# Kernel optimization log

Hardware: AMD Instinct MI355X
Metric: run time of the kernel (lower is better)

## Reference

```python
import jax, jax.numpy as jnp
import numpy as np

EPS = 1e-5  # torch BatchNorm2d default eps
NUM_PIXELS = 2  # M_Relax window
GROUPS = 4


def conv2d(x, w, b, groups, pad):
    y = jax.lax.conv_general_dilated(
        x, w, window_strides=(1, 1), padding=[(pad, pad), (pad, pad)],
        dimension_numbers=('NCHW', 'OIHW', 'NCHW'), feature_group_count=groups)
    return y + b[None, :, None, None]


def batchnorm(x, gamma, beta):
    # training-mode BN: batch statistics over (N,H,W)
    mean = jnp.mean(x, axis=(0, 2, 3), keepdims=True)
    var = jnp.var(x, axis=(0, 2, 3), keepdims=True)
    return gamma[None, :, None, None] * (x - mean) * jax.lax.rsqrt(var + EPS) + beta[None, :, None, None]


def resb(x, w1, b1, w2, b2):
    y = conv2d(x, w1, b1, GROUPS, 1)
    y = jnp.where(y > 0, y, 0.1 * y)  # LeakyReLU(0.1)
    y = conv2d(y, w2, b2, GROUPS, 1)
    return y + x


def m_relax(M, n=NUM_PIXELS):
    # sum of M shifted by -n..n along the query (row) axis with zero padding
    out = M
    for i in range(1, n + 1):
        out = out + jnp.pad(M[:, :-i, :], ((0, 0), (i, 0), (0, 0)))
        out = out + jnp.pad(M[:, i:, :], ((0, 0), (0, i), (0, 0)))
    return out


def reference(x_left, x_right, bn_gamma, bn_beta, rb_w1, rb_b1, rb_w2, rb_b2, q_w, q_b, k_w, k_b):
    b, c, h, w = x_left.shape
    Q = conv2d(resb(batchnorm(x_left, bn_gamma, bn_beta), rb_w1, rb_b1, rb_w2, rb_b2), q_w, q_b, GROUPS, 0)
    K = conv2d(resb(batchnorm(x_right, bn_gamma, bn_beta), rb_w1, rb_b1, rb_w2, rb_b2), k_w, k_b, GROUPS, 0)
    Q = Q - jnp.mean(Q, axis=3, keepdims=True)
    K = K - jnp.mean(K, axis=3, keepdims=True)
    # rows of each image attend across width: [b*h, w, c]
    Qr = Q.transpose(0, 2, 3, 1).reshape(b * h, w, c)
    Kr = K.transpose(0, 2, 3, 1).reshape(b * h, w, c)
    score = jnp.einsum('nuc,nvc->nuv', Qr, Kr)  # [b*h, w, w]
    M_rl = jax.nn.softmax(score, axis=-1)               # right->left
    M_lr = jax.nn.softmax(score.transpose(0, 2, 1), axis=-1)  # left->right
    # validity maps (detached in original)
    V_left = jax.lax.stop_gradient(jnp.einsum('nuv,nvu->nu', m_relax(M_rl), M_lr)).reshape(b, 1, h, w)
    V_right = jax.lax.stop_gradient(jnp.einsum('nuv,nvu->nu', m_relax(M_lr), M_rl)).reshape(b, 1, h, w)
    Vl = jnp.tanh(5.0 * V_left)
    Vr = jnp.tanh(5.0 * V_right)
    xr_rows = x_right.transpose(0, 2, 3, 1).reshape(b * h, w, c)
    xl_rows = x_left.transpose(0, 2, 3, 1).reshape(b * h, w, c)
    x_leftT = jnp.einsum('nuv,nvc->nuc', M_rl, xr_rows).reshape(b, h, w, c).transpose(0, 3, 1, 2)
    x_rightT = jnp.einsum('nuv,nvc->nuc', M_lr, xl_rows).reshape(b, h, w, c).transpose(0, 3, 1, 2)
    out_left = x_left * (1 - Vl) + x_leftT * Vl
    out_right = x_right * (1 - Vr) + x_rightT * Vr
    return out_left, out_right


def setup_inputs() -> dict:
    key = jax.random.key(0)
    ks = jax.random.split(key, 12)
    b, c, h, w = 8, 64, 128, 128
    cg = c // GROUPS
    s_conv3 = 0.1
    return {
        'x_left': jax.random.normal(ks[0], (b, c, h, w), jnp.float32),
        'x_right': jax.random.normal(ks[1], (b, c, h, w), jnp.float32),
        'bn_gamma': jnp.ones((c,), jnp.float32),
        'bn_beta': jnp.zeros((c,), jnp.float32),
        'rb_w1': jax.random.normal(ks[2], (c, cg, 3, 3), jnp.float32) * s_conv3,
        'rb_b1': jax.random.normal(ks[3], (c,), jnp.float32) * 0.01,
        'rb_w2': jax.random.normal(ks[4], (c, cg, 3, 3), jnp.float32) * s_conv3,
        'rb_b2': jax.random.normal(ks[5], (c,), jnp.float32) * 0.01,
        'q_w': jax.random.normal(ks[6], (c, cg, 1, 1), jnp.float32) * 0.2,
        'q_b': jax.random.normal(ks[7], (c,), jnp.float32) * 0.01,
        'k_w': jax.random.normal(ks[8], (c, cg, 1, 1), jnp.float32) * 0.2,
        'k_b': jax.random.normal(ks[9], (c,), jnp.float32) * 0.01,
    }
```

## Files before the change

kernel.cpp:

```cpp
#include <hip/hip_runtime.h>

#define CH_N 64
#define HH 128
#define WW 128
#define BB 8
#define HW (HH*WW)

__global__ __launch_bounds__(256) void k_stats(const float* __restrict__ xL,
                                               const float* __restrict__ xR,
                                               float* __restrict__ sums) {
  int blk = blockIdx.x;
  int img = blk >> 8, c = (blk >> 2) & 63, s = blk & 3;
  const float* x = img ? xR : xL;
  float sm = 0.f, sq = 0.f;
  for (int n = 2*s; n < 2*s+2; ++n) {
    const float4* p = (const float4*)(x + ((size_t)(n*64+c))*HW);
    for (int i = threadIdx.x; i < 4096; i += 256) {
      float4 v = p[i];
      sm += (v.x+v.y)+(v.z+v.w);
      sq += (v.x*v.x+v.y*v.y)+(v.z*v.z+v.w*v.w);
    }
  }
  #pragma unroll
  for (int o = 32; o > 0; o >>= 1) { sm += __shfl_down(sm, o); sq += __shfl_down(sq, o); }
  __shared__ float rs[2][4];
  int wid = threadIdx.x >> 6;
  if ((threadIdx.x & 63) == 0) { rs[0][wid] = sm; rs[1][wid] = sq; }
  __syncthreads();
  if (threadIdx.x == 0) {
    sm = (rs[0][0]+rs[0][1])+(rs[0][2]+rs[0][3]);
    sq = (rs[1][0]+rs[1][1])+(rs[1][2]+rs[1][3]);
    atomicAdd(&sums[(img*64+c)*2+0], sm);
    atomicAdd(&sums[(img*64+c)*2+1], sq);
  }
}

__global__ __launch_bounds__(128) void k_finalize(const float* __restrict__ sums,
                                                  const float* __restrict__ gamma,
                                                  const float* __restrict__ beta,
                                                  float* __restrict__ ss) {
  int t = threadIdx.x;
  if (t < 128) {
    int c = t & 63;
    float sm = sums[t*2], sq = sums[t*2+1];
    float mean = sm * (1.f/131072.f);
    float var  = sq * (1.f/131072.f) - mean*mean;
    float scale = gamma[c] * rsqrtf(var + 1e-5f);
    ss[t*2+0] = scale;
    ss[t*2+1] = beta[c] - mean*scale;
  }
}

#define WOFF  5760
#define QWOFF 4224
#define QBOFF 4480

template<int MODE>
__global__ __launch_bounds__(256, 4) void k_conv(
    const float* __restrict__ inL, const float* __restrict__ inR,
    const float* __restrict__ xresL, const float* __restrict__ xresR,
    const float* __restrict__ w, const float* __restrict__ bias,
    const float* __restrict__ ss,
    float* __restrict__ outL_, float* __restrict__ outR_,
    const float* __restrict__ qwL, const float* __restrict__ qbL,
    const float* __restrict__ qwR, const float* __restrict__ qbR,
    float* __restrict__ rsL, float* __restrict__ rsR) {
  __shared__ float smem[8832];
  int tile = blockIdx.x, g = blockIdx.y, nz = blockIdx.z;
  int img = nz >> 3, n = nz & 7;
  const float* in   = img ? inR : inL;
  const float* xres = img ? xresR : xresL;
  const float* ssp  = ss + img*128;
  float* out        = img ? outR_ : outL_;
  const float* qw1  = img ? qwR : qwL;
  const float* qb1  = img ? qbR : qbL;
  float* rowsum     = img ? rsR : rsL;

  int x0 = (tile & 7) << 4, y0 = (tile >> 3) << 4;
  int t = threadIdx.x;

  {
    int ocw = t >> 4, icw = t & 15;
    const float* wp = w + (size_t)(g*16 + ocw)*144 + icw*9;
    float* wd = &smem[WOFF + ocw*192 + icw*12];
    #pragma unroll
    for (int k = 0; k < 9; ++k) wd[k] = wp[k];
  }

  {
    int p0 = t, p1 = t + 256;
    int ry0 = p0 / 18, rx0 = p0 - ry0*18;
    int gy0 = y0 - 1 + ry0, gx0 = x0 - 1 + rx0;
    bool ok0 = ((unsigned)gy0 < 128u) && ((unsigned)gx0 < 128u);
    int gy0c = gy0 < 0 ? 0 : (gy0 > 127 ? 127 : gy0);
    int gx0c = gx0 < 0 ? 0 : (gx0 > 127 ? 127 : gx0);
    const float* sp0 = in + ((size_t)(n*64 + g*16)*128 + gy0c)*128 + gx0c;
    float* dp0 = &smem[ry0*20 + rx0];

    bool two = (p1 < 324);
    int ry1 = p1 / 18, rx1 = p1 - ry1*18;
    int gy1 = y0 - 1 + ry1, gx1 = x0 - 1 + rx1;
    bool ok1 = ((unsigned)gy1 < 128u) && ((unsigned)gx1 < 128u);
    int gy1c = gy1 < 0 ? 0 : (gy1 > 127 ? 127 : gy1);
    int gx1c = gx1 < 0 ? 0 : (gx1 > 127 ? 127 : gx1);
    const float* sp1 = in + ((size_t)(n*64 + g*16)*128 + gy1c)*128 + gx1c;
    float* dp1 = &smem[ry1*20 + rx1];

    #pragma unroll
    for (int ic = 0; ic < 16; ++ic) {
      float sA = 0.f, sB = 0.f;
      if (MODE == 0) { sA = ssp[(g*16+ic)*2]; sB = ssp[(g*16+ic)*2+1]; }
      float v0 = sp0[(size_t)ic*HW];
      if (MODE == 0) v0 = fmaf(v0, sA, sB);
      dp0[ic*360] = ok0 ? v0 : 0.f;
      if (two) {
        float v1 = sp1[(size_t)ic*HW];
        if (MODE == 0) v1 = fmaf(v1, sA, sB);
        dp1[ic*360] = ok1 ? v1 : 0.f;
      }
    }
  }
  __syncthreads();

  int oc = t >> 4, sub = t & 15;
  int sy = (sub >> 2) << 2, sx = (sub & 3) << 2;
  int c = g*16 + oc;
  float acc[4][4];
  float bv = bias[c];
  #pragma unroll
  for (int i = 0; i < 4; ++i)
    #pragma unroll
    for (int j = 0; j < 4; ++j) acc[i][j] = bv;

  for (int ic = 0; ic < 16; ++ic) {
    const float* it = &smem[ic*360 + sy*20 + sx];
    float win[6][6];
    #pragma unroll
    for (int r = 0; r < 6; ++r) {
      const float4 wa = *(const float4*)&it[r*20];
      const float2 wb = *(const float2*)&it[r*20 + 4];
      win[r][0]=wa.x; win[r][1]=wa.y; win[r][2]=wa.z; win[r][3]=wa.w;
      win[r][4]=wb.x; win[r][5]=wb.y;
    }
    const float4 w0 = *(const float4*)&smem[WOFF + oc*192 + ic*12];
    const float4 w1 = *(const float4*)&smem[WOFF + oc*192 + ic*12 + 4];
    const float  w8 = smem[WOFF + oc*192 + ic*12 + 8];
    float wv[9] = {w0.x,w0.y,w0.z,w0.w,w1.x,w1.y,w1.z,w1.w,w8};
    #pragma unroll
    for (int i = 0; i < 4; ++i)
      #pragma unroll
      for (int j = 0; j < 4; ++j) {
        float a = acc[i][j];
        #pragma unroll
        for (int ky = 0; ky < 3; ++ky)
          #pragma unroll
          for (int kx = 0; kx < 3; ++kx)
            a = fmaf(win[i+ky][j+kx], wv[ky*3+kx], a);
        acc[i][j] = a;
      }
  }

  if (MODE == 0) {
    #pragma unroll
    for (int i = 0; i < 4; ++i) {
      int oy = y0 + sy + i;
      size_t rowbase = ((size_t)(n*64+c)*128 + oy)*128;
      float4 o;
      o.x = acc[i][0] > 0.f ? acc[i][0] : 0.1f*acc[i][0];
      o.y = acc[i][1] > 0.f ? acc[i][1] : 0.1f*acc[i][1];
      o.z = acc[i][2] > 0.f ? acc[i][2] : 0.1f*acc[i][2];
      o.w = acc[i][3] > 0.f ? acc[i][3] : 0.1f*acc[i][3];
      *(float4*)&out[rowbase + x0 + sx] = o;
    }
  } else {
    float sA = ssp[c*2], sB = ssp[c*2+1];
    __syncthreads();
    #pragma unroll
    for (int i = 0; i < 4; ++i) {
      int oy = y0 + sy + i;
      size_t rowbase = ((size_t)(n*64+c)*128 + oy)*128;
      const float4 xr4 = *(const float4*)&xres[rowbase + x0 + sx];
      float4 v4;
      v4.x = acc[i][0] + fmaf(xr4.x, sA, sB);
      v4.y = acc[i][1] + fmaf(xr4.y, sA, sB);
      v4.z = acc[i][2] + fmaf(xr4.z, sA, sB);
      v4.w = acc[i][3] + fmaf(xr4.w, sA, sB);
      *(float4*)&smem[oc*264 + (sy+i)*16 + sx] = v4;
    }
    smem[QWOFF + t] = qw1[g*256 + t];
    if (t < 16) smem[QBOFF + t] = qb1[g*16 + t];
    __syncthreads();

    float qa[4][4];
    float bq = smem[QBOFF + oc];
    #pragma unroll
    for (int i = 0; i < 4; ++i)
      #pragma unroll
      for (int j = 0; j < 4; ++j) qa[i][j] = bq;
    #pragma unroll 4
    for (int ic = 0; ic < 16; ++ic) {
      float wq = smem[QWOFF + oc*16 + ic];
      #pragma unroll
      for (int i = 0; i < 4; ++i) {
        const float4 yv = *(const float4*)&smem[ic*264 + (sy+i)*16 + sx];
        qa[i][0] = fmaf(wq, yv.x, qa[i][0]);
        qa[i][1] = fmaf(wq, yv.y, qa[i][1]);
        qa[i][2] = fmaf(wq, yv.z, qa[i][2]);
        qa[i][3] = fmaf(wq, yv.w, qa[i][3]);
      }
    }
    #pragma unroll
    for (int i = 0; i < 4; ++i) {
      int oy = y0 + sy + i;
      size_t rowbase = ((size_t)(n*64+c)*128 + oy)*128;
      float4 o4 = make_float4(qa[i][0], qa[i][1], qa[i][2], qa[i][3]);
      *(float4*)&out[rowbase + x0 + sx] = o4;
      float r = (qa[i][0]+qa[i][1]) + (qa[i][2]+qa[i][3]);
      r += __shfl_xor(r, 1);
      r += __shfl_xor(r, 2);
      if ((t & 3) == 0) atomicAdd(&rowsum[(size_t)(n*64+c)*128 + oy], r);
    }
  }
}

__device__ __forceinline__ int SW(int r, int c) {
  return (r << 7) + (((c >> 2) ^ (r & 31)) << 2) + (c & 3);
}
__device__ __forceinline__ int SWQ(int r, int q) {
  return (r << 7) + ((q ^ (r & 31)) << 2);
}

__global__ __launch_bounds__(512, 4) void k_pam(const float* Q,
                                                const float* K,
                                                const float* __restrict__ XL,
                                                const float* __restrict__ XR,
                                                float* outL,
                                                float* outR,
                                                const float* __restrict__ rsL,
                                                const float* __restrict__ rsR) {
  extern __shared__ float smp[];
  float* ST   = smp;
  float* CHB  = smp + 16384;
  float* rmax = smp + 18432;
  float* rinv = rmax + 128;
  float* cmax = rmax + 256;
  float* cinv = rmax + 384;
  float* Vl   = rmax + 512;
  float* Vr   = rmax + 640;
  float* Pu   = rmax + 768;
  float* Qv   = rmax + 896;
  float* ms   = rmax + 1024;
  float* pm   = CHB;
  float* pl   = CHB + 512;
  float* pm2  = CHB + 1024;
  float* pl2  = CHB + 1536;

  int t = threadIdx.x;
  int b = blockIdx.x >> 7, h = blockIdx.x & 127;
  size_t qbase = ((size_t)(b*64)*128 + h)*128;

  {
    int u0 = (t & 31) << 2, v0 = (t >> 5) << 3;
    float a0[8], a1[8], a2[8], a3[8];
    #pragma unroll
    for (int j = 0; j < 8; ++j) { a0[j]=0.f; a1[j]=0.f; a2[j]=0.f; a3[j]=0.f; }
    int half = t >> 8;
    int cl_ld = (t >> 5) & 7;
    int u4_ld = (t & 31) << 2;
    const float* src = half ? K : Q;
    const float* rsum = half ? rsR : rsL;
    for (int cb = 0; cb < 8; ++cb) {
      float mean = rsum[((size_t)b*64 + cb*8 + cl_ld)*128 + h] * (1.f/128.f);
      __syncthreads();
      float4 v = *(const float4*)&src[qbase + (size_t)(cb*8 + cl_ld)*HW + u4_ld];
      v.x -= mean; v.y -= mean; v.z -= mean; v.w -= mean;
      *(float4*)&CHB[half*1024 + cl_ld*128 + u4_ld] = v;
      __syncthreads();
      #pragma unroll
      for (int cl = 0; cl < 8; ++cl) {
        const float4 qv = *(const float4*)&CHB[cl*128 + u0];
        const float4 k0 = *(const float4*)&CHB[1024 + cl*128 + v0];
        const float4 k1 = *(const float4*)&CHB[1024 + cl*128 + v0 + 4];
        float kk[8] = {k0.x,k0.y,k0.z,k0.w,k1.x,k1.y,k1.z,k1.w};
        #pragma unroll
        for (int j = 0; j < 8; ++j) {
          float kv = kk[j];
          a0[j] = fmaf(qv.x, kv, a0[j]);
          a1[j] = fmaf(qv.y, kv, a1[j]);
          a2[j] = fmaf(qv.z, kv, a2[j]);
          a3[j] = fmaf(qv.w, kv, a3[j]);
        }
      }
    }
    #pragma unroll
    for (int j = 0; j < 8; ++j) {
      int r = v0 + j;
      *(float4*)&ST[SWQ(r, u0 >> 2)] = make_float4(a0[j], a1[j], a2[j], a3[j]);
    }
  }
  __syncthreads();

  {
    int u = t & 127, q = t >> 7, vb = q << 5;
    float m = -1e30f;
    for (int v = vb; v < vb+32; ++v) m = fmaxf(m, ST[SW(v, u)]);
    float l = 0.f;
    for (int v = vb; v < vb+32; ++v) l += __expf(ST[SW(v, u)] - m);
    float m2 = -1e30f;
    for (int k = (vb >> 2); k < (vb >> 2) + 8; ++k) {
      const float4 x4 = *(const float4*)&ST[SWQ(u, k)];
      m2 = fmaxf(m2, fmaxf(fmaxf(x4.x, x4.y), fmaxf(x4.z, x4.w)));
    }
    float l2 = 0.f;
    for (int k = (vb >> 2); k < (vb >> 2) + 8; ++k) {
      const float4 x4 = *(const float4*)&ST[SWQ(u, k)];
      l2 += (__expf(x4.x-m2)+__expf(x4.y-m2)) + (__expf(x4.z-m2)+__expf(x4.w-m2));
    }
    pm[t] = m; pl[t] = l;
    pm2[t] = m2; pl2[t] = l2;
  }
  __syncthreads();
  if (t < 256) {
    int u = t & 127;
    const float* PM = (t < 128) ? pm : pm2;
    const float* PL = (t < 128) ? pl : pl2;
    float m = fmaxf(fmaxf(PM[u], PM[128+u]), fmaxf(PM[256+u], PM[384+u]));
    float l = PL[u]*__expf(PM[u]-m) + PL[128+u]*__expf(PM[128+u]-m)
            + PL[256+u]*__expf(PM[256+u]-m) + PL[384+u]*__expf(PM[384+u]-m);
    if (t < 128) { rmax[u] = m; rinv[u] = 1.f/l; }
    else         { cmax[u] = m; cinv[u] = 1.f/l; }
  }
  __syncthreads();

  if (t < 64) {
    float m = fmaxf(rmax[t], rmax[t+64]);
    #pragma unroll
    for (int o = 32; o > 0; o >>= 1) m = fmaxf(m, __shfl_down(m, o));
    if (t == 0) ms[0] = m;
  }
  __syncthreads();

  {
    float ms0 = ms[0];
    if (t < 128)      Pu[t] = __expf(rmax[t] - ms0) / rinv[t];
    else if (t < 256) { int v = t - 128; Qv[v] = __expf(ms0 - cmax[v]) * cinv[v]; }
    int u = t & 127, q = t >> 7;
    float ru = rmax[u], ri = rinv[u];
    for (int v = (q << 5); v < (q << 5) + 32; ++v) {
      int a = SW(v, u);
      ST[a] = __expf(ST[a] - ru) * ri;
    }
  }
  __syncthreads();

  {
    int u = t & 127, q = t >> 7, vb = q << 5;
    int rcl[5]; float wL[5], qvd[5];
    #pragma unroll
    for (int d = 0; d < 5; ++d) {
      int uu = u - 2 + d;
      bool ok = (uu >= 0 && uu < 128);
      rcl[d] = ok ? uu : u;
      wL[d]  = ok ? 1.f : 0.f;
      qvd[d] = ok ? Qv[uu] : 0.f;
    }
    float pu_u = Pu[u];
    float accL = 0.f, accR = 0.f;
    for (int v = vb; v < vb+32; ++v) {
      float rr0 = ST[SW(v, rcl[0])], rr1 = ST[SW(v, rcl[1])];
      float rr2 = ST[SW(v, u)];
      float rr3 = ST[SW(v, rcl[3])], rr4 = ST[SW(v, rcl[4])];
      float R = rr2 + (wL[0]*rr0 + wL[1]*rr1) + (wL[3]*rr3 + wL[4]*rr4);
      accL = fmaf(R * rr2, Qv[v], accL);
    }
    accL *= pu_u;
    {
      int ush = u >> 3;
      #pragma unroll 2
      for (int a = 0; a < 8; ++a) {
        #pragma unroll
        for (int bq = 0; bq < 4; ++bq) {
          int v = vb + (a << 2) + ((bq + ush) & 3);
          float cc0 = ST[SW(rcl[0], v)], cc1 = ST[SW(rcl[1], v)];
          float cc2 = ST[SW(u, v)];
          float cc3 = ST[SW(rcl[3], v)], cc4 = ST[SW(rcl[4], v)];
          float G = cc2*qvd[2] + (cc0*qvd[0] + cc1*qvd[1]) + (cc3*qvd[3] + cc4*qvd[4]);
          accR = fmaf(G * cc2, Pu[v], accR);
        }
      }
    }
    __syncthreads();
    pm[t] = accL; pl[t] = accR;
  }
  __syncthreads();
  if (t < 128) {
    float vsL = pm[t]+pm[128+t]+pm[256+t]+pm[384+t];
    float vsR = pl[t]+pl[128+t]+pl[256+t]+pl[384+t];
    Vl[t] = tanhf(5.f*vsL);
    Vr[t] = tanhf(5.f*vsR);
  }

  int ul = t & 63, c0 = (t >> 6) << 3;
  int c_ld = t >> 3, q_ld = (t & 7) << 2;
  int csw_st = c_ld ^ (((q_ld >> 2) & 7) << 3);

  {
    float acc0[8], acc1[8];
    #pragma unroll
    for (int j = 0; j < 8; ++j) { acc0[j]=0.f; acc1[j]=0.f; }
    for (int cb = 0; cb < 4; ++cb) {
      int vb = cb << 5;
      __syncthreads();
      {
        const float4 r4 = *(const float4*)&XR[qbase + (size_t)c_ld*HW + vb + q_ld];
        CHB[(q_ld+0)*64+csw_st] = r4.x; CHB[(q_ld+1)*64+csw_st] = r4.y;
        CHB[(q_ld+2)*64+csw_st] = r4.z; CHB[(q_ld+3)*64+csw_st] = r4.w;
      }
      __syncthreads();
      for (int vv = 0; vv < 32; ++vv) {
        int v = vb + vv;
        float m0 = ST[SW(v, ul)];
        float m1 = ST[SW(v, ul+64)];
        int cs = c0 ^ (((vv >> 2) & 7) << 3);
        const float4 xa = *(const float4*)&CHB[vv*64 + cs];
        const float4 xb = *(const float4*)&CHB[vv*64 + cs + 4];
        acc0[0]=fmaf(m0,xa.x,acc0[0]); acc0[1]=fmaf(m0,xa.y,acc0[1]);
        acc0[2]=fmaf(m0,xa.z,acc0[2]); acc0[3]=fmaf(m0,xa.w,acc0[3]);
        acc0[4]=fmaf(m0,xb.x,acc0[4]); acc0[5]=fmaf(m0,xb.y,acc0[5]);
        acc0[6]=fmaf(m0,xb.z,acc0[6]); acc0[7]=fmaf(m0,xb.w,acc0[7]);
        acc1[0]=fmaf(m1,xa.x,acc1[0]); acc1[1]=fmaf(m1,xa.y,acc1[1]);
        acc1[2]=fmaf(m1,xa.z,acc1[2]); acc1[3]=fmaf(m1,xa.w,acc1[3]);
        acc1[4]=fmaf(m1,xb.x,acc1[4]); acc1[5]=fmaf(m1,xb.y,acc1[5]);
        acc1[6]=fmaf(m1,xb.z,acc1[6]); acc1[7]=fmaf(m1,xb.w,acc1[7]);
      }
    }
    float vl0 = Vl[ul], vl1 = Vl[ul+64];
    #pragma unroll
    for (int j = 0; j < 8; ++j) {
      size_t o0 = qbase + (size_t)(c0+j)*HW + ul;
      outL[o0]    = XL[o0]   *(1.f-vl0) + acc0[j]*vl0;
      outL[o0+64] = XL[o0+64]*(1.f-vl1) + acc1[j]*vl1;
    }
  }

  {
    float acc0[8], acc1[8];
    #pragma unroll
    for (int j = 0; j < 8; ++j) { acc0[j]=0.f; acc1[j]=0.f; }
    float qv_u0 = Qv[ul], qv_u1 = Qv[ul+64];
    for (int cb = 0; cb < 4; ++cb) {
      int vb = cb << 5, qb = cb << 3;
      __syncthreads();
      {
        const float4 r4 = *(const float4*)&XL[qbase + (size_t)c_ld*HW + vb + q_ld];
        CHB[(q_ld+0)*64+csw_st] = r4.x; CHB[(q_ld+1)*64+csw_st] = r4.y;
        CHB[(q_ld+2)*64+csw_st] = r4.z; CHB[(q_ld+3)*64+csw_st] = r4.w;
      }
      __syncthreads();
      for (int lq = 0; lq < 8; ++lq) {
        const float4 s0 = *(const float4*)&ST[SWQ(ul,    qb+lq)];
        const float4 s1 = *(const float4*)&ST[SWQ(ul+64, qb+lq)];
        const float4 pu4 = *(const float4*)&Pu[(qb+lq) << 2];
        float sv0[4] = {s0.x, s0.y, s0.z, s0.w};
        float sv1[4] = {s1.x, s1.y, s1.z, s1.w};
        float pv[4]  = {pu4.x, pu4.y, pu4.z, pu4.w};
        int cs = c0 ^ ((lq & 7) << 3);
        #pragma unroll
        for (int k = 0; k < 4; ++k) {
          float m0 = sv0[k] * pv[k] * qv_u0;
          float m1 = sv1[k] * pv[k] * qv_u1;
          const float4 xa0 = *(const float4*)&CHB[((lq<<2)+k)*64 + cs];
          const float4 xb0 = *(const float4*)&CHB[((lq<<2)+k)*64 + cs + 4];
          acc0[0]=fmaf(m0,xa0.x,acc0[0]); acc0[1]=fmaf(m0,xa0.y,acc0[1]);
          acc0[2]=fmaf(m0,xa0.z,acc0[2]); acc0[3]=fmaf(m0,xa0.w,acc0[3]);
          acc0[4]=fmaf(m0,xb0.x,acc0[4]); acc0[5]=fmaf(m0,xb0.y,acc0[5]);
          acc0[6]=fmaf(m0,xb0.z,acc0[6]); acc0[7]=fmaf(m0,xb0.w,acc0[7]);
          acc1[0]=fmaf(m1,xa0.x,acc1[0]); acc1[1]=fmaf(m1,xa0.y,acc1[1]);
          acc1[2]=fmaf(m1,xa0.z,acc1[2]); acc1[3]=fmaf(m1,xa0.w,acc1[3]);
          acc1[4]=fmaf(m1,xb0.x,acc1[4]); acc1[5]=fmaf(m1,xb0.y,acc1[5]);
          acc1[6]=fmaf(m1,xb0.z,acc1[6]); acc1[7]=fmaf(m1,xb0.w,acc1[7]);
        }
      }
    }
    float vr0 = Vr[ul], vr1 = Vr[ul+64];
    #pragma unroll
    for (int j = 0; j < 8; ++j) {
      size_t o0 = qbase + (size_t)(c0+j)*HW + ul;
      outR[o0]    = XR[o0]   *(1.f-vr0) + acc0[j]*vr0;
      outR[o0+64] = XR[o0+64]*(1.f-vr1) + acc1[j]*vr1;
    }
  }
}

extern "C" void kernel_launch(void* const* d_in, const int* in_sizes, int n_in,
                              void* d_out, int out_size, void* d_ws, size_t ws_size,
                              hipStream_t stream) {
  const float* xL    = (const float*)d_in[0];
  const float* xR    = (const float*)d_in[1];
  const float* gamma = (const float*)d_in[2];
  const float* beta  = (const float*)d_in[3];
  const float* rw1   = (const float*)d_in[4];
  const float* rb1   = (const float*)d_in[5];
  const float* rw2   = (const float*)d_in[6];
  const float* rb2   = (const float*)d_in[7];
  const float* qw    = (const float*)d_in[8];
  const float* qb    = (const float*)d_in[9];
  const float* kw    = (const float*)d_in[10];
  const float* kb    = (const float*)d_in[11];
  float* out = (float*)d_out;
  char* ws = (char*)d_ws;

  const size_t BUF = (size_t)BB*CH_N*HW*4;
  float* y1L  = (float*)(ws);
  float* y1R  = (float*)(ws + BUF);
  float* sums = (float*)(ws + 2*BUF);
  float* ss   = sums + 256;
  float* rsL  = sums + 512;
  float* rsR  = rsL + (size_t)BB*CH_N*HH;

  float* Qb = out;
  float* Kb = out + (size_t)BB*CH_N*HW;

  hipMemsetAsync(sums, 0, (512 + 2*(size_t)BB*CH_N*HH)*sizeof(float), stream);
  k_stats<<<512, 256, 0, stream>>>(xL, xR, sums);
  k_finalize<<<1, 128, 0, stream>>>(sums, gamma, beta, ss);

  dim3 cg(64, 4, 16);
  k_conv<0><<<cg, 256, 0, stream>>>(xL, xR, xL, xR, rw1, rb1, ss, y1L, y1R,
                                    nullptr, nullptr, nullptr, nullptr, nullptr, nullptr);
  k_conv<1><<<cg, 256, 0, stream>>>(y1L, y1R, xL, xR, rw2, rb2, ss, Qb, Kb,
                                    qw, qb, kw, kb, rsL, rsR);

  const int SMEM = 19464 * 4;
  hipFuncSetAttribute((const void*)k_pam, hipFuncAttributeMaxDynamicSharedMemorySize, SMEM);
  k_pam<<<1024, 512, SMEM, stream>>>(Qb, Kb, xL, xR, Qb, Kb, rsL, rsR);
}
```

Before: 549.0 us.

## Prefetch next chunk in registers in k_pam and de-alias Q/K from outputs

In k_pam, the global loads for the next channel or column chunk of Q/K, XR and XL are issued before the barrier, so they overlap with the shared-memory compute on the current chunk. Q and K move into a separate workspace buffer, with K reusing the y1L space, so they no longer alias the outputs. This lets k_pam's pointers be marked __restrict__. The second conv is split into two launches, one per image, each with the weights bound directly. Costs are extra register pressure from the prefetched values, one more kernel launch, and a larger workspace requirement.

```diff
diff --git a/kernel.cpp b/kernel.cpp
--- a/kernel.cpp
+++ b/kernel.cpp
@@ -63,8 +63,7 @@
     const float* __restrict__ ss,
     float* __restrict__ outL_, float* __restrict__ outR_,
     const float* __restrict__ qwL, const float* __restrict__ qbL,
-    const float* __restrict__ qwR, const float* __restrict__ qbR,
-    float* __restrict__ rsL, float* __restrict__ rsR) {
+    float* __restrict__ rsL) {
   __shared__ float smem[8832];
   int tile = blockIdx.x, g = blockIdx.y, nz = blockIdx.z;
   int img = nz >> 3, n = nz & 7;
@@ -72,9 +71,9 @@
   const float* xres = img ? xresR : xresL;
   const float* ssp  = ss + img*128;
   float* out        = img ? outR_ : outL_;
-  const float* qw1  = img ? qwR : qwL;
-  const float* qb1  = img ? qbR : qbL;
-  float* rowsum     = img ? rsR : rsL;
+  const float* qw1  = qwL;
+  const float* qb1  = qbL;
+  float* rowsum     = rsL;
 
   int x0 = (tile & 7) << 4, y0 = (tile >> 3) << 4;
   int t = threadIdx.x;
@@ -230,12 +229,12 @@
   return (r << 7) + ((q ^ (r & 31)) << 2);
 }
 
-__global__ __launch_bounds__(512, 4) void k_pam(const float* Q,
-                                                const float* K,
+__global__ __launch_bounds__(512, 4) void k_pam(const float* __restrict__ Q,
+                                                const float* __restrict__ K,
                                                 const float* __restrict__ XL,
                                                 const float* __restrict__ XR,
-                                                float* outL,
-                                                float* outR,
+                                                float* __restrict__ outL,
+                                                float* __restrict__ outR,
                                                 const float* __restrict__ rsL,
                                                 const float* __restrict__ rsR) {
   extern __shared__ float smp[];
@@ -269,12 +268,16 @@
     int u4_ld = (t & 31) << 2;
     const float* src = half ? K : Q;
     const float* rsum = half ? rsR : rsL;
+    float mean = rsum[((size_t)b*64 + cl_ld)*128 + h] * (1.f/128.f);
+    float4 v = *(const float4*)&src[qbase + (size_t)cl_ld*HW + u4_ld];
     for (int cb = 0; cb < 8; ++cb) {
-      float mean = rsum[((size_t)b*64 + cb*8 + cl_ld)*128 + h] * (1.f/128.f);
       __syncthreads();
-      float4 v = *(const float4*)&src[qbase + (size_t)(cb*8 + cl_ld)*HW + u4_ld];
       v.x -= mean; v.y -= mean; v.z -= mean; v.w -= mean;
       *(float4*)&CHB[half*1024 + cl_ld*128 + u4_ld] = v;
+      if (cb < 7) {
+        mean = rsum[((size_t)b*64 + (cb+1)*8 + cl_ld)*128 + h] * (1.f/128.f);
+        v = *(const float4*)&src[qbase + (size_t)((cb+1)*8 + cl_ld)*HW + u4_ld];
+      }
       __syncthreads();
       #pragma unroll
       for (int cl = 0; cl < 8; ++cl) {
@@ -408,15 +411,15 @@
     float acc0[8], acc1[8];
     #pragma unroll
     for (int j = 0; j < 8; ++j) { acc0[j]=0.f; acc1[j]=0.f; }
+    float4 r4 = *(const float4*)&XR[qbase + (size_t)c_ld*HW + q_ld];
     for (int cb = 0; cb < 4; ++cb) {
+      __syncthreads();
+      CHB[(q_ld+0)*64+csw_st] = r4.x; CHB[(q_ld+1)*64+csw_st] = r4.y;
+      CHB[(q_ld+2)*64+csw_st] = r4.z; CHB[(q_ld+3)*64+csw_st] = r4.w;
+      if (cb < 3)
+        r4 = *(const float4*)&XR[qbase + (size_t)c_ld*HW + ((cb+1) << 5) + q_ld];
+      __syncthreads();
       int vb = cb << 5;
-      __syncthreads();
-      {
-        const float4 r4 = *(const float4*)&XR[qbase + (size_t)c_ld*HW + vb + q_ld];
-        CHB[(q_ld+0)*64+csw_st] = r4.x; CHB[(q_ld+1)*64+csw_st] = r4.y;
-        CHB[(q_ld+2)*64+csw_st] = r4.z; CHB[(q_ld+3)*64+csw_st] = r4.w;
-      }
-      __syncthreads();
       for (int vv = 0; vv < 32; ++vv) {
         int v = vb + vv;
         float m0 = ST[SW(v, ul)];
@@ -448,15 +451,15 @@
     #pragma unroll
     for (int j = 0; j < 8; ++j) { acc0[j]=0.f; acc1[j]=0.f; }
     float qv_u0 = Qv[ul], qv_u1 = Qv[ul+64];
+    float4 r4 = *(const float4*)&XL[qbase + (size_t)c_ld*HW + q_ld];
     for (int cb = 0; cb < 4; ++cb) {
-      int vb = cb << 5, qb = cb << 3;
       __syncthreads();
-      {
-        const float4 r4 = *(const float4*)&XL[qbase + (size_t)c_ld*HW + vb + q_ld];
-        CHB[(q_ld+0)*64+csw_st] = r4.x; CHB[(q_ld+1)*64+csw_st] = r4.y;
-        CHB[(q_ld+2)*64+csw_st] = r4.z; CHB[(q_ld+3)*64+csw_st] = r4.w;
-      }
+      CHB[(q_ld+0)*64+csw_st] = r4.x; CHB[(q_ld+1)*64+csw_st] = r4.y;
+      CHB[(q_ld+2)*64+csw_st] = r4.z; CHB[(q_ld+3)*64+csw_st] = r4.w;
+      if (cb < 3)
+        r4 = *(const float4*)&XL[qbase + (size_t)c_ld*HW + ((cb+1) << 5) + q_ld];
       __syncthreads();
+      int qb = cb << 3;
       for (int lq = 0; lq < 8; ++lq) {
         const float4 s0 = *(const float4*)&ST[SWQ(ul,    qb+lq)];
         const float4 s1 = *(const float4*)&ST[SWQ(ul+64, qb+lq)];
@@ -513,25 +516,27 @@
   const size_t BUF = (size_t)BB*CH_N*HW*4;
   float* y1L  = (float*)(ws);
   float* y1R  = (float*)(ws + BUF);
-  float* sums = (float*)(ws + 2*BUF);
+  float* Qb   = (float*)(ws + 2*BUF);
+  float* Kb   = y1L;
+  float* sums = (float*)(ws + 3*BUF);
   float* ss   = sums + 256;
   float* rsL  = sums + 512;
   float* rsR  = rsL + (size_t)BB*CH_N*HH;
 
-  float* Qb = out;
-  float* Kb = out + (size_t)BB*CH_N*HW;
-
   hipMemsetAsync(sums, 0, (512 + 2*(size_t)BB*CH_N*HH)*sizeof(float), stream);
   k_stats<<<512, 256, 0, stream>>>(xL, xR, sums);
   k_finalize<<<1, 128, 0, stream>>>(sums, gamma, beta, ss);
 
-  dim3 cg(64, 4, 16);
-  k_conv<0><<<cg, 256, 0, stream>>>(xL, xR, xL, xR, rw1, rb1, ss, y1L, y1R,
-                                    nullptr, nullptr, nullptr, nullptr, nullptr, nullptr);
-  k_conv<1><<<cg, 256, 0, stream>>>(y1L, y1R, xL, xR, rw2, rb2, ss, Qb, Kb,
-                                    qw, qb, kw, kb, rsL, rsR);
+  dim3 cg0(64, 4, 16);
+  k_conv<0><<<cg0, 256, 0, stream>>>(xL, xR, xL, xR, rw1, rb1, ss, y1L, y1R,
+                                     nullptr, nullptr, nullptr);
+  dim3 cg1(64, 4, 8);
+  k_conv<1><<<cg1, 256, 0, stream>>>(y1L, nullptr, xL, nullptr, rw2, rb2, ss,
+                                     Qb, nullptr, qw, qb, rsL);
+  k_conv<1><<<cg1, 256, 0, stream>>>(y1R, nullptr, xR, nullptr, rw2, rb2, ss + 128,
+                                     Kb, nullptr, kw, kb, rsR);
 
   const int SMEM = 19464 * 4;
   hipFuncSetAttribute((const void*)k_pam, hipFuncAttributeMaxDynamicSharedMemorySize, SMEM);
-  k_pam<<<1024, 512, SMEM, stream>>>(Qb, Kb, xL, xR, Qb, Kb, rsL, rsR);
-}
+  k_pam<<<1024, 512, SMEM, stream>>>(Qb, Kb, xL, xR, out, out + (size_t)BB*CH_N*HW, rsL, rsR);
+}
```

After: 573.8 us. 4.5% more time.
